# Performance work log

Measured on AMD Instinct MI355X. Metric: run time of the kernel, lower is better.

## Reference

```python
import jax, jax.numpy as jnp
import numpy as np

N_NODES = 100000
N_EDGES = 1600000
IN_DIM, H1, H2, OUT_DIM = 128, 64, 64, 64


def _glorot(key, shape):
    fan_in, fan_out = shape
    lim = np.sqrt(6.0 / (fan_in + fan_out)).astype(np.float32)
    return jax.random.uniform(key, shape, jnp.float32, -lim, lim)


def setup_inputs() -> dict:
    key = jax.random.key(0)
    ks = jax.random.split(key, 8)
    x = jax.random.normal(ks[0], (N_NODES, IN_DIM), jnp.float32)
    edge_index = jax.random.randint(ks[1], (2, N_EDGES), 0, N_NODES, jnp.int64)
    W1 = _glorot(ks[2], (IN_DIM, H1))
    b1 = jnp.zeros((H1,), jnp.float32)
    W2 = _glorot(ks[3], (H1, H2))
    b2 = jnp.zeros((H2,), jnp.float32)
    Wfc = _glorot(ks[4], (H2, OUT_DIM))
    bfc = jnp.zeros((OUT_DIM,), jnp.float32)
    return {"x": x, "W1": W1, "b1": b1, "W2": W2, "b2": b2,
            "Wfc": Wfc, "bfc": bfc, "edge_index": edge_index}


def _gcn_conv(x, src, dst, dinv, W, b, n_nodes):
    # PyG GCNConv: h = D^{-1/2} (A + I) D^{-1/2} (x W) + b
    h = x @ W                                   # [N, out]
    norm = dinv[src] * dinv[dst]                # [E'] edge weights
    msg = norm[:, None] * h[src]                # gather + scale, [E', out]
    agg = jax.ops.segment_sum(msg, dst, num_segments=n_nodes)
    return agg + b


def reference(x, W1, b1, W2, b2, Wfc, bfc, edge_index):
    n = x.shape[0]
    loop = jnp.arange(n, dtype=edge_index.dtype)
    src = jnp.concatenate([edge_index[0], loop])   # self-loops appended
    dst = jnp.concatenate([edge_index[1], loop])
    deg = jnp.zeros((n,), x.dtype).at[dst].add(1.0)  # degree incl. self-loop
    dinv = jax.lax.rsqrt(deg)

    h = jax.nn.relu(_gcn_conv(x, src, dst, dinv, W1, b1, n))
    h = jax.nn.relu(_gcn_conv(h, src, dst, dinv, W2, b2, n))
    embedding = h
    logits = h @ Wfc + bfc
    return embedding, logits
```

## Files before the change

### kernel.cpp

```cpp
#include <hip/hip_runtime.h>
#include <hip/hip_bf16.h>


constexpr int IN_DIM  = 128;
constexpr int HDIM    = 64;
constexpr int NBLK_A  = 256;
constexpr int BSH     = 8;
constexpr int MAXNB   = 512;
constexpr int PADSLK  = 1792;

__device__ __forceinline__ float bf2f(unsigned int u) {
    return __uint_as_float(u << 16);
}
__device__ __forceinline__ unsigned short f2bf_bits(float f) {
    __hip_bfloat16 b = __float2bfloat16(f);
    return *(unsigned short*)&b;
}


__global__ void binA_count(const int* __restrict__ dst, int* __restrict__ histg,
                           int E, int NB, int chunk) {
    __shared__ int h[MAXNB];
    for (int i = threadIdx.x; i < NB; i += 256) h[i] = 0;
    __syncthreads();
    int beg = blockIdx.x * chunk;
    int end = min(E, beg + chunk);
    for (int e = beg + threadIdx.x; e < end; e += 256)
        atomicAdd(&h[dst[e] >> BSH], 1);
    __syncthreads();
    for (int i = threadIdx.x; i < NB; i += 256)
        histg[i * NBLK_A + blockIdx.x] = h[i];
}

__global__ void binA_scanblocks(int* __restrict__ histg, int* __restrict__ btot) {
    __shared__ int sm[NBLK_A];
    int tid = threadIdx.x;
    int v = histg[blockIdx.x * NBLK_A + tid];
    sm[tid] = v;
    __syncthreads();
    for (int off = 1; off < NBLK_A; off <<= 1) {
        int t = (tid >= off) ? sm[tid - off] : 0;
        __syncthreads();
        sm[tid] += t;
        __syncthreads();
    }
    histg[blockIdx.x * NBLK_A + tid] = sm[tid] - v;
    if (tid == NBLK_A - 1) btot[blockIdx.x] = sm[tid];
}

__device__ __forceinline__ void bucket_scan(const int* __restrict__ btot,
                                            int* bb, int NB) {
    int tid = threadIdx.x;
    for (int i = tid; i < MAXNB; i += 256) bb[i] = (i < NB) ? btot[i] : 0;
    __syncthreads();
    for (int off = 1; off < MAXNB; off <<= 1) {
        int i0 = tid, i1 = tid + 256;
        int t0 = (i0 >= off) ? bb[i0 - off] : 0;
        int t1 = (i1 >= off) ? bb[i1 - off] : 0;
        __syncthreads();
        bb[i0] += t0;
        bb[i1] += t1;
        __syncthreads();
    }
}

__global__ void binA_scatter(const int* __restrict__ src, const int* __restrict__ dst,
                             const int* __restrict__ histg, const int* __restrict__ btot,
                             int* __restrict__ staging, int E, int NB, int chunk) {
    __shared__ int bb[MAXNB];
    __shared__ int cur[MAXNB];
    bucket_scan(btot, bb, NB);
    for (int i = threadIdx.x; i < NB; i += 256)
        cur[i] = (bb[i] - btot[i]) + histg[i * NBLK_A + blockIdx.x];
    __syncthreads();
    int beg = blockIdx.x * chunk;
    int end = min(E, beg + chunk);
    for (int e = beg + threadIdx.x; e < end; e += 256) {
        int s = src[e];
        int d = dst[e];
        int pos = atomicAdd(&cur[d >> BSH], 1);
        staging[pos] = (s << BSH) | (d & 255);
    }
}

__global__ void binB_finalize(const int* __restrict__ staging, const int* __restrict__ btot,
                              int2* __restrict__ rows, int* __restrict__ esrc,
                              float* __restrict__ dinv, unsigned int* __restrict__ hp_rowN,
                              int N, int NB) {
    __shared__ int bb[MAXNB];
    __shared__ int cnt[256], sm[256], cur[256];
    int tid = threadIdx.x;
    int b = blockIdx.x;
    bucket_scan(btot, bb, NB);
    int node0 = b << BSH;
    int nloc = min(256, N - node0);
    int eend = bb[b];
    int ebeg = eend - btot[b];
    int ebegP = ebeg + b * PADSLK;
    cnt[tid] = 0;
    __syncthreads();
    for (int e = ebeg + tid; e < eend; e += 256)
        atomicAdd(&cnt[staging[e] & 255], 1);
    __syncthreads();
    int v = cnt[tid];
    int pv = (v + 7) & ~7;
    sm[tid] = pv;
    __syncthreads();
    for (int off = 1; off < 256; off <<= 1) {
        int t = (tid >= off) ? sm[tid - off] : 0;
        __syncthreads();
        sm[tid] += t;
        __syncthreads();
    }
    int excl = sm[tid] - pv;
    cur[tid] = excl;
    __syncthreads();
    if (tid < nloc) {
        rows[node0 + tid] = make_int2(ebegP + excl, ebegP + excl + pv);
        dinv[node0 + tid] = rsqrtf((float)v + 1.0f);
        for (int q = v; q < pv; ++q)
            esrc[ebegP + excl + q] = N;
    }
    if (b == 0 && tid < 32) hp_rowN[tid] = 0u;
    for (int e = ebeg + tid; e < eend; e += 256) {
        int p = staging[e];
        int pos = ebegP + atomicAdd(&cur[p & 255], 1);
        esrc[pos] = p >> BSH;
    }
}


template<int K, bool IBF16, bool SCALE, bool BIAS, bool OBF16>
__device__ __forceinline__ void gemm_body(
        const void* __restrict__ Xv, const float* __restrict__ W,
        const float* __restrict__ bias, const float* __restrict__ dinv,
        void* __restrict__ Yv, int n) {
    constexpr int KC = 32;
    constexpr int XSTR = 132;
    __shared__ float Xt[KC * XSTR];
    __shared__ float Ws[KC * 64];
    const int tid = threadIdx.x;
    const int node0 = blockIdx.x * 128;
    const int r0 = (tid >> 4) * 8;
    const int c0 = (tid & 15) * 4;

    float acc[8][4];
#pragma unroll
    for (int a = 0; a < 8; ++a)
#pragma unroll
        for (int b = 0; b < 4; ++b) acc[a][b] = 0.f;

    for (int kc = 0; kc < K; kc += KC) {
        __syncthreads();
#pragma unroll
        for (int i = 0; i < 4; ++i) {
            int s = tid + i * 256;
            int row = s >> 3;
            int kq = s & 7;
            int grow = node0 + row;
            float4 v = make_float4(0.f, 0.f, 0.f, 0.f);
            if (grow < n) {
                if (IBF16) {
                    uint2 u = *(const uint2*)&((const unsigned short*)Xv)[(size_t)grow * K + kc + kq * 4];
                    v.x = bf2f(u.x & 0xffff); v.y = bf2f(u.x >> 16);
                    v.z = bf2f(u.y & 0xffff); v.w = bf2f(u.y >> 16);
                } else {
                    v = *(const float4*)&((const float*)Xv)[(size_t)grow * K + kc + kq * 4];
                }
            }
            Xt[(kq * 4 + 0) * XSTR + row] = v.x;
            Xt[(kq * 4 + 1) * XSTR + row] = v.y;
            Xt[(kq * 4 + 2) * XSTR + row] = v.z;
            Xt[(kq * 4 + 3) * XSTR + row] = v.w;
        }
#pragma unroll
        for (int i = 0; i < 2; ++i) {
            int s = tid + i * 256;
            *(float4*)&Ws[s * 4] = *(const float4*)&W[(size_t)kc * 64 + s * 4];
        }
        __syncthreads();
#pragma unroll
        for (int kk = 0; kk < KC; kk += 4) {
            float4 xa[4][2];
            float4 wv[4];
#pragma unroll
            for (int i = 0; i < 4; ++i) {
                xa[i][0] = *(const float4*)&Xt[(kk + i) * XSTR + r0];
                xa[i][1] = *(const float4*)&Xt[(kk + i) * XSTR + r0 + 4];
                wv[i]    = *(const float4*)&Ws[(kk + i) * 64 + c0];
            }
#pragma unroll
            for (int i = 0; i < 4; ++i) {
                const float* xp = (const float*)&xa[i][0];
                const float* wp = (const float*)&wv[i];
#pragma unroll
                for (int rr = 0; rr < 8; ++rr)
#pragma unroll
                    for (int cc = 0; cc < 4; ++cc)
                        acc[rr][cc] += xp[rr] * wp[cc];
            }
        }
    }
#pragma unroll
    for (int rr = 0; rr < 8; ++rr) {
        int node = node0 + r0 + rr;
        if (node < n) {
            float d = SCALE ? dinv[node] : 1.0f;
            float t[4];
#pragma unroll
            for (int cc = 0; cc < 4; ++cc) {
                float v = acc[rr][cc];
                if (BIAS) v += bias[c0 + cc];
                t[cc] = v * d;
            }
            if (OBF16) {
                __hip_bfloat16 vb[4];
#pragma unroll
                for (int cc = 0; cc < 4; ++cc) vb[cc] = __float2bfloat16(t[cc]);
                *(uint2*)&((__hip_bfloat16*)Yv)[(size_t)node * 64 + c0] = *(uint2*)vb;
            } else {
                *(float4*)&((float*)Yv)[(size_t)node * 64 + c0] = *(float4*)t;
            }
        }
    }
}

__global__ __launch_bounds__(256, 4) void gemm1_kernel(
        const float* X, const float* W, const float* dinv, void* Y, int n) {
    gemm_body<IN_DIM, false, true, false, true>(X, W, nullptr, dinv, Y, n);
}
__global__ __launch_bounds__(256, 4) void gemm2_kernel(
        const void* X, const float* W, const float* dinv, void* Y, int n) {
    gemm_body<HDIM, true, true, false, true>(X, W, nullptr, dinv, Y, n);
}
__global__ __launch_bounds__(256, 4) void fc_kernel(
        const float* X, const float* W, const float* bias, void* Y, int n) {
    gemm_body<HDIM, false, false, true, false>(X, W, bias, nullptr, Y, n);
}

template<bool OBF16>
__global__ __launch_bounds__(256) void agg_kernel(
        const uint4* __restrict__ hp4, const int* __restrict__ esrc,
        const int2* __restrict__ rows, const float* __restrict__ dinv,
        const float* __restrict__ bias, void* __restrict__ out, int n) {
    const int lane = threadIdx.x & 63;
    const int j = lane & 7;
    const int step = gridDim.x * 32;
    for (int idx = blockIdx.x * 32 + (threadIdx.x >> 6) * 8 + (lane >> 3);
         idx < n; idx += step) {
        const int node = idx;
        const int2 be = rows[node];

        float acc[8];
        {
            uint4 u = hp4[(size_t)node * 8 + j];
            acc[0] = bf2f(u.x & 0xffff); acc[1] = bf2f(u.x >> 16);
            acc[2] = bf2f(u.y & 0xffff); acc[3] = bf2f(u.y >> 16);
            acc[4] = bf2f(u.z & 0xffff); acc[5] = bf2f(u.z >> 16);
            acc[6] = bf2f(u.w & 0xffff); acc[7] = bf2f(u.w >> 16);
        }
        int k = be.x;
        for (; k + 16 <= be.y; k += 16) {
            int s[16];
#pragma unroll
            for (int i = 0; i < 16; ++i)
                s[i] = __builtin_nontemporal_load(&esrc[k + i]);
            uint4 u[16];
#pragma unroll
            for (int i = 0; i < 16; ++i)
                u[i] = hp4[(size_t)s[i] * 8 + j];
#pragma unroll
            for (int i = 0; i < 16; ++i) {
                acc[0] += bf2f(u[i].x & 0xffff); acc[1] += bf2f(u[i].x >> 16);
                acc[2] += bf2f(u[i].y & 0xffff); acc[3] += bf2f(u[i].y >> 16);
                acc[4] += bf2f(u[i].z & 0xffff); acc[5] += bf2f(u[i].z >> 16);
                acc[6] += bf2f(u[i].w & 0xffff); acc[7] += bf2f(u[i].w >> 16);
            }
        }
        if (k < be.y) {
            int s[8];
#pragma unroll
            for (int i = 0; i < 8; ++i)
                s[i] = __builtin_nontemporal_load(&esrc[k + i]);
            uint4 u[8];
#pragma unroll
            for (int i = 0; i < 8; ++i)
                u[i] = hp4[(size_t)s[i] * 8 + j];
#pragma unroll
            for (int i = 0; i < 8; ++i) {
                acc[0] += bf2f(u[i].x & 0xffff); acc[1] += bf2f(u[i].x >> 16);
                acc[2] += bf2f(u[i].y & 0xffff); acc[3] += bf2f(u[i].y >> 16);
                acc[4] += bf2f(u[i].z & 0xffff); acc[5] += bf2f(u[i].z >> 16);
                acc[6] += bf2f(u[i].w & 0xffff); acc[7] += bf2f(u[i].w >> 16);
            }
        }
        const float d = dinv[node];
        float o[8];
#pragma unroll
        for (int t = 0; t < 8; ++t)
            o[t] = fmaxf(fmaf(d, acc[t], bias[8 * j + t]), 0.f);

        if (OBF16) {
            uint4 pk;
            pk.x = (unsigned)f2bf_bits(o[0]) | ((unsigned)f2bf_bits(o[1]) << 16);
            pk.y = (unsigned)f2bf_bits(o[2]) | ((unsigned)f2bf_bits(o[3]) << 16);
            pk.z = (unsigned)f2bf_bits(o[4]) | ((unsigned)f2bf_bits(o[5]) << 16);
            pk.w = (unsigned)f2bf_bits(o[6]) | ((unsigned)f2bf_bits(o[7]) << 16);
            ((uint4*)out)[(size_t)node * 8 + j] = pk;
        } else {
            ((float4*)out)[(size_t)node * 16 + 2 * j]     = make_float4(o[0], o[1], o[2], o[3]);
            ((float4*)out)[(size_t)node * 16 + 2 * j + 1] = make_float4(o[4], o[5], o[6], o[7]);
        }
    }
}

extern "C" void kernel_launch(void* const* d_in, const int* in_sizes, int n_in,
                              void* d_out, int out_size, void* d_ws, size_t ws_size,
                              hipStream_t stream) {
    const float* x   = (const float*)d_in[0];
    const float* W1  = (const float*)d_in[1];
    const float* b1  = (const float*)d_in[2];
    const float* W2  = (const float*)d_in[3];
    const float* b2  = (const float*)d_in[4];
    const float* Wfc = (const float*)d_in[5];
    const float* bfc = (const float*)d_in[6];
    const int*  eidx = (const int*)d_in[7];

    const int N = in_sizes[0] / IN_DIM;
    const int E = in_sizes[7] / 2;
    const int* src = eidx;
    const int* dst = eidx + E;

    const int NB    = (N + 255) >> BSH;
    const int chunk = (E + NBLK_A - 1) / NBLK_A;
    const int EP    = E + NB * PADSLK;

    int* p = (int*)d_ws;
    int2* rows = (int2*)p;           p += (size_t)2 * N + 2;
    float* dinv = (float*)p;         p += (size_t)((N + 3) & ~3);
    int* histg = p;                  p += (size_t)((NB * NBLK_A + 3) & ~3);
    int* btot = p;                   p += 512;
    int* esrc = p;                   p += (size_t)((EP + 3) & ~3);
    unsigned short* hp = (unsigned short*)p;   p += (size_t)(N + 1) * 32;
    unsigned short* h1 = (unsigned short*)p;   p += (size_t)N * 32;
    int* staging = (int*)hp;
    unsigned int* hp_rowN = (unsigned int*)(hp + (size_t)N * 64);

    float* emb    = (float*)d_out;
    float* logits = emb + (size_t)N * HDIM;

    binA_count<<<NBLK_A, 256, 0, stream>>>(dst, histg, E, NB, chunk);
    binA_scanblocks<<<NB, NBLK_A, 0, stream>>>(histg, btot);
    binA_scatter<<<NBLK_A, 256, 0, stream>>>(src, dst, histg, btot, staging, E, NB, chunk);
    binB_finalize<<<NB, 256, 0, stream>>>(staging, btot, rows, esrc, dinv, hp_rowN, N, NB);

    const int gBlocks = (N + 127) / 128;
    const int aBlocks = 2048;

    gemm1_kernel<<<gBlocks, 256, 0, stream>>>(x, W1, dinv, hp, N);
    agg_kernel<true><<<aBlocks, 256, 0, stream>>>(
        (const uint4*)hp, esrc, rows, dinv, b1, h1, N);

    gemm2_kernel<<<gBlocks, 256, 0, stream>>>(h1, W2, dinv, hp, N);
    agg_kernel<false><<<aBlocks, 256, 0, stream>>>(
        (const uint4*)hp, esrc, rows, dinv, b2, emb, N);

    fc_kernel<<<gBlocks, 256, 0, stream>>>(emb, Wfc, bfc, logits, N);
}
```

Measured before the change: 314.8 us.

## Fuse next-layer GEMM and FC into aggregation kernels

The layer-2 GEMM and the final FC layer are folded into the epilogues of the two aggregation kernels. Each 8-lane group writes its aggregated row to shared memory and multiplies it by a weight matrix held in LDS, which removes two kernel launches and the round trips of h1 and the embedding through global memory. A second padded bf16 buffer is added for layer-2 features, and the 16-wide unrolled gather loop is dropped in favour of the 8-wide one. The cost is 16KB+ of shared memory per block, which may reduce occupancy of the memory-bound gather, plus redundant per-node matmul work done on CUDA cores.

```diff
diff --git a/kernel.cpp b/kernel.cpp
--- a/kernel.cpp
+++ b/kernel.cpp
@@ -86,7 +86,7 @@
 __global__ void binB_finalize(const int* __restrict__ staging, const int* __restrict__ btot,
                               int2* __restrict__ rows, int* __restrict__ esrc,
                               float* __restrict__ dinv, unsigned int* __restrict__ hp_rowN,
-                              int N, int NB) {
+                              unsigned int* __restrict__ hp2_rowN, int N, int NB) {
     __shared__ int bb[MAXNB];
     __shared__ int cnt[256], sm[256], cur[256];
     int tid = threadIdx.x;
@@ -121,7 +121,10 @@
         for (int q = v; q < pv; ++q)
             esrc[ebegP + excl + q] = N;
     }
-    if (b == 0 && tid < 32) hp_rowN[tid] = 0u;
+    if (b == 0 && tid < 32) {
+        hp_rowN[tid] = 0u;
+        hp2_rowN[tid] = 0u;
+    }
     for (int e = ebeg + tid; e < eend; e += 256) {
         int p = staging[e];
         int pos = ebegP + atomicAdd(&cur[p & 255], 1);
@@ -130,11 +133,10 @@
 }
 
 
-template<int K, bool IBF16, bool SCALE, bool BIAS, bool OBF16>
-__device__ __forceinline__ void gemm_body(
-        const void* __restrict__ Xv, const float* __restrict__ W,
-        const float* __restrict__ bias, const float* __restrict__ dinv,
-        void* __restrict__ Yv, int n) {
+__global__ __launch_bounds__(256, 4) void gemm1_kernel(
+        const float* __restrict__ X, const float* __restrict__ W,
+        const float* __restrict__ dinv, unsigned short* __restrict__ Y, int n) {
+    constexpr int K = IN_DIM;
     constexpr int KC = 32;
     constexpr int XSTR = 132;
     __shared__ float Xt[KC * XSTR];
@@ -159,15 +161,8 @@
             int kq = s & 7;
             int grow = node0 + row;
             float4 v = make_float4(0.f, 0.f, 0.f, 0.f);
-            if (grow < n) {
-                if (IBF16) {
-                    uint2 u = *(const uint2*)&((const unsigned short*)Xv)[(size_t)grow * K + kc + kq * 4];
-                    v.x = bf2f(u.x & 0xffff); v.y = bf2f(u.x >> 16);
-                    v.z = bf2f(u.y & 0xffff); v.w = bf2f(u.y >> 16);
-                } else {
-                    v = *(const float4*)&((const float*)Xv)[(size_t)grow * K + kc + kq * 4];
-                }
-            }
+            if (grow < n)
+                v = *(const float4*)&X[(size_t)grow * K + kc + kq * 4];
             Xt[(kq * 4 + 0) * XSTR + row] = v.x;
             Xt[(kq * 4 + 1) * XSTR + row] = v.y;
             Xt[(kq * 4 + 2) * XSTR + row] = v.z;
@@ -205,79 +200,56 @@
     for (int rr = 0; rr < 8; ++rr) {
         int node = node0 + r0 + rr;
         if (node < n) {
-            float d = SCALE ? dinv[node] : 1.0f;
-            float t[4];
-#pragma unroll
-            for (int cc = 0; cc < 4; ++cc) {
-                float v = acc[rr][cc];
-                if (BIAS) v += bias[c0 + cc];
-                t[cc] = v * d;
-            }
-            if (OBF16) {
-                __hip_bfloat16 vb[4];
-#pragma unroll
-                for (int cc = 0; cc < 4; ++cc) vb[cc] = __float2bfloat16(t[cc]);
-                *(uint2*)&((__hip_bfloat16*)Yv)[(size_t)node * 64 + c0] = *(uint2*)vb;
-            } else {
-                *(float4*)&((float*)Yv)[(size_t)node * 64 + c0] = *(float4*)t;
-            }
-        }
-    }
-}
-
-__global__ __launch_bounds__(256, 4) void gemm1_kernel(
-        const float* X, const float* W, const float* dinv, void* Y, int n) {
-    gemm_body<IN_DIM, false, true, false, true>(X, W, nullptr, dinv, Y, n);
-}
-__global__ __launch_bounds__(256, 4) void gemm2_kernel(
-        const void* X, const float* W, const float* dinv, void* Y, int n) {
-    gemm_body<HDIM, true, true, false, true>(X, W, nullptr, dinv, Y, n);
-}
-__global__ __launch_bounds__(256, 4) void fc_kernel(
-        const float* X, const float* W, const float* bias, void* Y, int n) {
-    gemm_body<HDIM, false, false, true, false>(X, W, bias, nullptr, Y, n);
-}
-
-template<bool OBF16>
-__global__ __launch_bounds__(256) void agg_kernel(
+            float d = dinv[node];
+            __hip_bfloat16 vb[4];
+#pragma unroll
+            for (int cc = 0; cc < 4; ++cc)
+                vb[cc] = __float2bfloat16(acc[rr][cc] * d);
+            *(uint2*)&Y[(size_t)node * 64 + c0] = *(uint2*)vb;
+        }
+    }
+}
+
+template<int MODE>
+__global__ __launch_bounds__(256) void agg_fused(
         const uint4* __restrict__ hp4, const int* __restrict__ esrc,
         const int2* __restrict__ rows, const float* __restrict__ dinv,
-        const float* __restrict__ bias, void* __restrict__ out, int n) {
+        const float* __restrict__ bias, const float* __restrict__ Wn,
+        const float* __restrict__ bfc, void* __restrict__ out,
+        float* __restrict__ logits, int n) {
+    __shared__ float Ws[64 * 64];
+    __shared__ float rb[4][8][68];
+    for (int i = threadIdx.x; i < 1024; i += 256)
+        ((float4*)Ws)[i] = ((const float4*)Wn)[i];
+    __syncthreads();
+
     const int lane = threadIdx.x & 63;
     const int j = lane & 7;
+    const int g = lane >> 3;
+    const int w = threadIdx.x >> 6;
     const int step = gridDim.x * 32;
-    for (int idx = blockIdx.x * 32 + (threadIdx.x >> 6) * 8 + (lane >> 3);
-         idx < n; idx += step) {
-        const int node = idx;
-        const int2 be = rows[node];
+
+    float bb0[8];
+#pragma unroll
+    for (int t = 0; t < 8; ++t) bb0[t] = bias[8 * j + t];
+    float bo[8];
+    if (MODE == 1) {
+#pragma unroll
+        for (int t = 0; t < 8; ++t) bo[t] = bfc[8 * j + t];
+    }
+
+    for (int idx = blockIdx.x * 32 + w * 8 + g; idx < n; idx += step) {
+        const int2 be = rows[idx];
 
         float acc[8];
         {
-            uint4 u = hp4[(size_t)node * 8 + j];
+            uint4 u = hp4[(size_t)idx * 8 + j];
             acc[0] = bf2f(u.x & 0xffff); acc[1] = bf2f(u.x >> 16);
             acc[2] = bf2f(u.y & 0xffff); acc[3] = bf2f(u.y >> 16);
             acc[4] = bf2f(u.z & 0xffff); acc[5] = bf2f(u.z >> 16);
             acc[6] = bf2f(u.w & 0xffff); acc[7] = bf2f(u.w >> 16);
         }
-        int k = be.x;
-        for (; k + 16 <= be.y; k += 16) {
-            int s[16];
-#pragma unroll
-            for (int i = 0; i < 16; ++i)
-                s[i] = __builtin_nontemporal_load(&esrc[k + i]);
-            uint4 u[16];
-#pragma unroll
-            for (int i = 0; i < 16; ++i)
-                u[i] = hp4[(size_t)s[i] * 8 + j];
-#pragma unroll
-            for (int i = 0; i < 16; ++i) {
-                acc[0] += bf2f(u[i].x & 0xffff); acc[1] += bf2f(u[i].x >> 16);
-                acc[2] += bf2f(u[i].y & 0xffff); acc[3] += bf2f(u[i].y >> 16);
-                acc[4] += bf2f(u[i].z & 0xffff); acc[5] += bf2f(u[i].z >> 16);
-                acc[6] += bf2f(u[i].w & 0xffff); acc[7] += bf2f(u[i].w >> 16);
-            }
-        }
-        if (k < be.y) {
+        for (int k = be.x; k < be.y; k += 8) {
             int s[8];
 #pragma unroll
             for (int i = 0; i < 8; ++i)
@@ -294,22 +266,47 @@
                 acc[6] += bf2f(u[i].w & 0xffff); acc[7] += bf2f(u[i].w >> 16);
             }
         }
-        const float d = dinv[node];
+        const float d = dinv[idx];
         float o[8];
 #pragma unroll
         for (int t = 0; t < 8; ++t)
-            o[t] = fmaxf(fmaf(d, acc[t], bias[8 * j + t]), 0.f);
-
-        if (OBF16) {
+            o[t] = fmaxf(fmaf(d, acc[t], bb0[t]), 0.f);
+
+        *(float4*)&rb[w][g][j * 8]     = make_float4(o[0], o[1], o[2], o[3]);
+        *(float4*)&rb[w][g][j * 8 + 4] = make_float4(o[4], o[5], o[6], o[7]);
+
+        float y[8] = {0.f, 0.f, 0.f, 0.f, 0.f, 0.f, 0.f, 0.f};
+#pragma unroll
+        for (int fw = 0; fw < 8; ++fw) {
+            float4 r0 = *(const float4*)&rb[w][g][fw * 8];
+            float4 r1 = *(const float4*)&rb[w][g][fw * 8 + 4];
+            float rv[8] = {r0.x, r0.y, r0.z, r0.w, r1.x, r1.y, r1.z, r1.w};
+#pragma unroll
+            for (int e = 0; e < 8; ++e) {
+                float val = rv[e];
+                const float4 w0 = *(const float4*)&Ws[(fw * 8 + e) * 64 + j * 8];
+                const float4 w1 = *(const float4*)&Ws[(fw * 8 + e) * 64 + j * 8 + 4];
+                y[0] = fmaf(val, w0.x, y[0]); y[1] = fmaf(val, w0.y, y[1]);
+                y[2] = fmaf(val, w0.z, y[2]); y[3] = fmaf(val, w0.w, y[3]);
+                y[4] = fmaf(val, w1.x, y[4]); y[5] = fmaf(val, w1.y, y[5]);
+                y[6] = fmaf(val, w1.z, y[6]); y[7] = fmaf(val, w1.w, y[7]);
+            }
+        }
+
+        if (MODE == 0) {
             uint4 pk;
-            pk.x = (unsigned)f2bf_bits(o[0]) | ((unsigned)f2bf_bits(o[1]) << 16);
-            pk.y = (unsigned)f2bf_bits(o[2]) | ((unsigned)f2bf_bits(o[3]) << 16);
-            pk.z = (unsigned)f2bf_bits(o[4]) | ((unsigned)f2bf_bits(o[5]) << 16);
-            pk.w = (unsigned)f2bf_bits(o[6]) | ((unsigned)f2bf_bits(o[7]) << 16);
-            ((uint4*)out)[(size_t)node * 8 + j] = pk;
+            pk.x = (unsigned)f2bf_bits(y[0] * d) | ((unsigned)f2bf_bits(y[1] * d) << 16);
+            pk.y = (unsigned)f2bf_bits(y[2] * d) | ((unsigned)f2bf_bits(y[3] * d) << 16);
+            pk.z = (unsigned)f2bf_bits(y[4] * d) | ((unsigned)f2bf_bits(y[5] * d) << 16);
+            pk.w = (unsigned)f2bf_bits(y[6] * d) | ((unsigned)f2bf_bits(y[7] * d) << 16);
+            ((uint4*)out)[(size_t)idx * 8 + j] = pk;
         } else {
-            ((float4*)out)[(size_t)node * 16 + 2 * j]     = make_float4(o[0], o[1], o[2], o[3]);
-            ((float4*)out)[(size_t)node * 16 + 2 * j + 1] = make_float4(o[4], o[5], o[6], o[7]);
+            ((float4*)out)[(size_t)idx * 16 + 2 * j]     = make_float4(o[0], o[1], o[2], o[3]);
+            ((float4*)out)[(size_t)idx * 16 + 2 * j + 1] = make_float4(o[4], o[5], o[6], o[7]);
+            float4 l0 = make_float4(y[0] + bo[0], y[1] + bo[1], y[2] + bo[2], y[3] + bo[3]);
+            float4 l1 = make_float4(y[4] + bo[4], y[5] + bo[5], y[6] + bo[6], y[7] + bo[7]);
+            *(float4*)&logits[(size_t)idx * 64 + 8 * j]     = l0;
+            *(float4*)&logits[(size_t)idx * 64 + 8 * j + 4] = l1;
         }
     }
 }
@@ -341,10 +338,11 @@
     int* histg = p;                  p += (size_t)((NB * NBLK_A + 3) & ~3);
     int* btot = p;                   p += 512;
     int* esrc = p;                   p += (size_t)((EP + 3) & ~3);
-    unsigned short* hp = (unsigned short*)p;   p += (size_t)(N + 1) * 32;
-    unsigned short* h1 = (unsigned short*)p;   p += (size_t)N * 32;
+    unsigned short* hp  = (unsigned short*)p;  p += (size_t)(N + 1) * 32;
+    unsigned short* hp2 = (unsigned short*)p;  p += (size_t)(N + 1) * 32;
     int* staging = (int*)hp;
-    unsigned int* hp_rowN = (unsigned int*)(hp + (size_t)N * 64);
+    unsigned int* hp_rowN  = (unsigned int*)(hp  + (size_t)N * 64);
+    unsigned int* hp2_rowN = (unsigned int*)(hp2 + (size_t)N * 64);
 
     float* emb    = (float*)d_out;
     float* logits = emb + (size_t)N * HDIM;
@@ -352,18 +350,17 @@
     binA_count<<<NBLK_A, 256, 0, stream>>>(dst, histg, E, NB, chunk);
     binA_scanblocks<<<NB, NBLK_A, 0, stream>>>(histg, btot);
     binA_scatter<<<NBLK_A, 256, 0, stream>>>(src, dst, histg, btot, staging, E, NB, chunk);
-    binB_finalize<<<NB, 256, 0, stream>>>(staging, btot, rows, esrc, dinv, hp_rowN, N, NB);
+    binB_finalize<<<NB, 256, 0, stream>>>(staging, btot, rows, esrc, dinv,
+                                          hp_rowN, hp2_rowN, N, NB);
 
     const int gBlocks = (N + 127) / 128;
     const int aBlocks = 2048;
 
     gemm1_kernel<<<gBlocks, 256, 0, stream>>>(x, W1, dinv, hp, N);
-    agg_kernel<true><<<aBlocks, 256, 0, stream>>>(
-        (const uint4*)hp, esrc, rows, dinv, b1, h1, N);
-
-    gemm2_kernel<<<gBlocks, 256, 0, stream>>>(h1, W2, dinv, hp, N);
-    agg_kernel<false><<<aBlocks, 256, 0, stream>>>(
-        (const uint4*)hp, esrc, rows, dinv, b2, emb, N);
-
-    fc_kernel<<<gBlocks, 256, 0, stream>>>(emb, Wfc, bfc, logits, N);
-}
+
+    agg_fused<0><<<aBlocks, 256, 0, stream>>>(
+        (const uint4*)hp, esrc, rows, dinv, b1, W2, nullptr, hp2, nullptr, N);
+
+    agg_fused<1><<<aBlocks, 256, 0, stream>>>(
+        (const uint4*)hp2, esrc, rows, dinv, b2, Wfc, bfc, emb, logits, N);
+}
```

Result: slower. 405.2 us (+28.7%).

## Replace two-level bucketed CSR build with atomic histogram and fused scatter

Applied to the files above, without the earlier changes.

Replaces the four-kernel bucket-sort CSR construction with a global degree histogram built by atomics, a wave-level scan that hands out row slots through an atomic counter, and an edge scatter using per-node atomic cursors. The scatter is folded into the first GEMM launch as extra blocks, so edge placement can overlap with the dense transform. Rows are no longer in node order and edges within a row land in nondeterministic order, which can hurt gather locality in aggregation and makes summation order vary between runs. Global atomics on 1.6M edges replace the shared-memory atomics used before.

```diff
diff --git a/kernel.cpp b/kernel.cpp
--- a/kernel.cpp
+++ b/kernel.cpp
@@ -4,10 +4,7 @@
 
 constexpr int IN_DIM  = 128;
 constexpr int HDIM    = 64;
-constexpr int NBLK_A  = 256;
-constexpr int BSH     = 8;
-constexpr int MAXNB   = 512;
-constexpr int PADSLK  = 1792;
+constexpr int SB      = 256;
 
 __device__ __forceinline__ float bf2f(unsigned int u) {
     return __uint_as_float(u << 16);
@@ -18,114 +15,44 @@
 }
 
 
-__global__ void binA_count(const int* __restrict__ dst, int* __restrict__ histg,
-                           int E, int NB, int chunk) {
-    __shared__ int h[MAXNB];
-    for (int i = threadIdx.x; i < NB; i += 256) h[i] = 0;
-    __syncthreads();
-    int beg = blockIdx.x * chunk;
-    int end = min(E, beg + chunk);
-    for (int e = beg + threadIdx.x; e < end; e += 256)
-        atomicAdd(&h[dst[e] >> BSH], 1);
-    __syncthreads();
-    for (int i = threadIdx.x; i < NB; i += 256)
-        histg[i * NBLK_A + blockIdx.x] = h[i];
-}
-
-__global__ void binA_scanblocks(int* __restrict__ histg, int* __restrict__ btot) {
-    __shared__ int sm[NBLK_A];
-    int tid = threadIdx.x;
-    int v = histg[blockIdx.x * NBLK_A + tid];
-    sm[tid] = v;
-    __syncthreads();
-    for (int off = 1; off < NBLK_A; off <<= 1) {
-        int t = (tid >= off) ? sm[tid - off] : 0;
-        __syncthreads();
-        sm[tid] += t;
-        __syncthreads();
-    }
-    histg[blockIdx.x * NBLK_A + tid] = sm[tid] - v;
-    if (tid == NBLK_A - 1) btot[blockIdx.x] = sm[tid];
-}
-
-__device__ __forceinline__ void bucket_scan(const int* __restrict__ btot,
-                                            int* bb, int NB) {
-    int tid = threadIdx.x;
-    for (int i = tid; i < MAXNB; i += 256) bb[i] = (i < NB) ? btot[i] : 0;
-    __syncthreads();
-    for (int off = 1; off < MAXNB; off <<= 1) {
-        int i0 = tid, i1 = tid + 256;
-        int t0 = (i0 >= off) ? bb[i0 - off] : 0;
-        int t1 = (i1 >= off) ? bb[i1 - off] : 0;
-        __syncthreads();
-        bb[i0] += t0;
-        bb[i1] += t1;
-        __syncthreads();
-    }
-}
-
-__global__ void binA_scatter(const int* __restrict__ src, const int* __restrict__ dst,
-                             const int* __restrict__ histg, const int* __restrict__ btot,
-                             int* __restrict__ staging, int E, int NB, int chunk) {
-    __shared__ int bb[MAXNB];
-    __shared__ int cur[MAXNB];
-    bucket_scan(btot, bb, NB);
-    for (int i = threadIdx.x; i < NB; i += 256)
-        cur[i] = (bb[i] - btot[i]) + histg[i * NBLK_A + blockIdx.x];
-    __syncthreads();
-    int beg = blockIdx.x * chunk;
-    int end = min(E, beg + chunk);
-    for (int e = beg + threadIdx.x; e < end; e += 256) {
-        int s = src[e];
-        int d = dst[e];
-        int pos = atomicAdd(&cur[d >> BSH], 1);
-        staging[pos] = (s << BSH) | (d & 255);
-    }
-}
-
-__global__ void binB_finalize(const int* __restrict__ staging, const int* __restrict__ btot,
-                              int2* __restrict__ rows, int* __restrict__ esrc,
-                              float* __restrict__ dinv, unsigned int* __restrict__ hp_rowN,
-                              int N, int NB) {
-    __shared__ int bb[MAXNB];
-    __shared__ int cnt[256], sm[256], cur[256];
-    int tid = threadIdx.x;
-    int b = blockIdx.x;
-    bucket_scan(btot, bb, NB);
-    int node0 = b << BSH;
-    int nloc = min(256, N - node0);
-    int eend = bb[b];
-    int ebeg = eend - btot[b];
-    int ebegP = ebeg + b * PADSLK;
-    cnt[tid] = 0;
-    __syncthreads();
-    for (int e = ebeg + tid; e < eend; e += 256)
-        atomicAdd(&cnt[staging[e] & 255], 1);
-    __syncthreads();
-    int v = cnt[tid];
-    int pv = (v + 7) & ~7;
-    sm[tid] = pv;
-    __syncthreads();
-    for (int off = 1; off < 256; off <<= 1) {
-        int t = (tid >= off) ? sm[tid - off] : 0;
-        __syncthreads();
-        sm[tid] += t;
-        __syncthreads();
-    }
-    int excl = sm[tid] - pv;
-    cur[tid] = excl;
-    __syncthreads();
-    if (tid < nloc) {
-        rows[node0 + tid] = make_int2(ebegP + excl, ebegP + excl + pv);
-        dinv[node0 + tid] = rsqrtf((float)v + 1.0f);
-        for (int q = v; q < pv; ++q)
-            esrc[ebegP + excl + q] = N;
-    }
-    if (b == 0 && tid < 32) hp_rowN[tid] = 0u;
-    for (int e = ebeg + tid; e < eend; e += 256) {
-        int p = staging[e];
-        int pos = ebegP + atomicAdd(&cur[p & 255], 1);
-        esrc[pos] = p >> BSH;
+__global__ void zero_kernel(int* __restrict__ deg, int* __restrict__ total,
+                            unsigned int* __restrict__ hp_rowN, int N) {
+    int i = blockIdx.x * 256 + threadIdx.x;
+    int step = gridDim.x * 256;
+    for (; i < N; i += step) deg[i] = 0;
+    if (blockIdx.x == 0 && threadIdx.x == 0) *total = 0;
+    if (blockIdx.x == 1 && threadIdx.x < 32) hp_rowN[threadIdx.x] = 0u;
+}
+
+__global__ void hist_kernel(const int* __restrict__ dst, int* __restrict__ deg, int E) {
+    int i = blockIdx.x * 256 + threadIdx.x;
+    int step = gridDim.x * 256;
+    for (; i < E; i += step) atomicAdd(&deg[dst[i]], 1);
+}
+
+__global__ void alloc_kernel(const int* __restrict__ deg, int* __restrict__ total,
+                             int2* __restrict__ rows, int* __restrict__ cur,
+                             float* __restrict__ dinv, int* __restrict__ esrc, int N) {
+    int idx = blockIdx.x * 256 + threadIdx.x;
+    int lane = threadIdx.x & 63;
+    int dg = (idx < N) ? deg[idx] : 0;
+    int pv = (dg + 7) & ~7;
+    int incl = pv;
+#pragma unroll
+    for (int off = 1; off < 64; off <<= 1) {
+        int t = __shfl_up(incl, off, 64);
+        if (lane >= off) incl += t;
+    }
+    int wtot = __shfl(incl, 63, 64);
+    int base = 0;
+    if (lane == 63) base = atomicAdd(total, wtot);
+    base = __shfl(base, 63, 64);
+    int start = base + incl - pv;
+    if (idx < N) {
+        rows[idx] = make_int2(start, start + pv);
+        cur[idx] = start;
+        dinv[idx] = rsqrtf((float)dg + 1.0f);
+        for (int q = dg; q < pv; ++q) esrc[start + q] = N;
     }
 }
 
@@ -134,13 +61,13 @@
 __device__ __forceinline__ void gemm_body(
         const void* __restrict__ Xv, const float* __restrict__ W,
         const float* __restrict__ bias, const float* __restrict__ dinv,
-        void* __restrict__ Yv, int n) {
+        void* __restrict__ Yv, int n, int bid) {
     constexpr int KC = 32;
     constexpr int XSTR = 132;
     __shared__ float Xt[KC * XSTR];
     __shared__ float Ws[KC * 64];
     const int tid = threadIdx.x;
-    const int node0 = blockIdx.x * 128;
+    const int node0 = bid * 128;
     const int r0 = (tid >> 4) * 8;
     const int c0 = (tid & 15) * 4;
 
@@ -225,18 +152,33 @@
     }
 }
 
-__global__ __launch_bounds__(256, 4) void gemm1_kernel(
-        const float* X, const float* W, const float* dinv, void* Y, int n) {
-    gemm_body<IN_DIM, false, true, false, true>(X, W, nullptr, dinv, Y, n);
-}
+__global__ __launch_bounds__(256, 4) void gemm1_scatter_kernel(
+        const float* __restrict__ X, const float* __restrict__ W,
+        const float* __restrict__ dinv, unsigned short* __restrict__ Y,
+        const int* __restrict__ src, const int* __restrict__ dst,
+        int* __restrict__ cur, int* __restrict__ esrc, int gB, int E, int n) {
+    if ((int)blockIdx.x >= gB) {
+        int i = ((int)blockIdx.x - gB) * 256 + threadIdx.x;
+        int step = SB * 256;
+        for (; i < E; i += step) {
+            int d = dst[i];
+            int p = atomicAdd(&cur[d], 1);
+            esrc[p] = src[i];
+        }
+        return;
+    }
+    gemm_body<IN_DIM, false, true, false, true>(X, W, nullptr, dinv, Y, n, blockIdx.x);
+}
+
 __global__ __launch_bounds__(256, 4) void gemm2_kernel(
         const void* X, const float* W, const float* dinv, void* Y, int n) {
-    gemm_body<HDIM, true, true, false, true>(X, W, nullptr, dinv, Y, n);
+    gemm_body<HDIM, true, true, false, true>(X, W, nullptr, dinv, Y, n, blockIdx.x);
 }
 __global__ __launch_bounds__(256, 4) void fc_kernel(
         const float* X, const float* W, const float* bias, void* Y, int n) {
-    gemm_body<HDIM, false, false, true, false>(X, W, bias, nullptr, Y, n);
-}
+    gemm_body<HDIM, false, false, true, false>(X, W, bias, nullptr, Y, n, blockIdx.x);
+}
+
 
 template<bool OBF16>
 __global__ __launch_bounds__(256) void agg_kernel(
@@ -331,39 +273,38 @@
     const int* src = eidx;
     const int* dst = eidx + E;
 
-    const int NB    = (N + 255) >> BSH;
-    const int chunk = (E + NBLK_A - 1) / NBLK_A;
-    const int EP    = E + NB * PADSLK;
+    const int EP = E + 7 * ((N + 7) & ~7) + 16;
 
     int* p = (int*)d_ws;
     int2* rows = (int2*)p;           p += (size_t)2 * N + 2;
     float* dinv = (float*)p;         p += (size_t)((N + 3) & ~3);
-    int* histg = p;                  p += (size_t)((NB * NBLK_A + 3) & ~3);
-    int* btot = p;                   p += 512;
+    int* deg = p;                    p += (size_t)((N + 3) & ~3);
+    int* cur = p;                    p += (size_t)((N + 3) & ~3);
+    int* total = p;                  p += 4;
     int* esrc = p;                   p += (size_t)((EP + 3) & ~3);
     unsigned short* hp = (unsigned short*)p;   p += (size_t)(N + 1) * 32;
     unsigned short* h1 = (unsigned short*)p;   p += (size_t)N * 32;
-    int* staging = (int*)hp;
     unsigned int* hp_rowN = (unsigned int*)(hp + (size_t)N * 64);
 
     float* emb    = (float*)d_out;
     float* logits = emb + (size_t)N * HDIM;
 
-    binA_count<<<NBLK_A, 256, 0, stream>>>(dst, histg, E, NB, chunk);
-    binA_scanblocks<<<NB, NBLK_A, 0, stream>>>(histg, btot);
-    binA_scatter<<<NBLK_A, 256, 0, stream>>>(src, dst, histg, btot, staging, E, NB, chunk);
-    binB_finalize<<<NB, 256, 0, stream>>>(staging, btot, rows, esrc, dinv, hp_rowN, N, NB);
-
-    const int gBlocks = (N + 127) / 128;
+    const int gB = (N + 127) / 128;
     const int aBlocks = 2048;
 
-    gemm1_kernel<<<gBlocks, 256, 0, stream>>>(x, W1, dinv, hp, N);
+    zero_kernel<<<256, 256, 0, stream>>>(deg, total, hp_rowN, N);
+    hist_kernel<<<512, 256, 0, stream>>>(dst, deg, E);
+    alloc_kernel<<<(N + 255) / 256, 256, 0, stream>>>(deg, total, rows, cur, dinv, esrc, N);
+
+    gemm1_scatter_kernel<<<gB + SB, 256, 0, stream>>>(
+        x, W1, dinv, hp, src, dst, cur, esrc, gB, E, N);
+
     agg_kernel<true><<<aBlocks, 256, 0, stream>>>(
         (const uint4*)hp, esrc, rows, dinv, b1, h1, N);
 
-    gemm2_kernel<<<gBlocks, 256, 0, stream>>>(h1, W2, dinv, hp, N);
+    gemm2_kernel<<<gB, 256, 0, stream>>>(h1, W2, dinv, hp, N);
     agg_kernel<false><<<aBlocks, 256, 0, stream>>>(
         (const uint4*)hp, esrc, rows, dinv, b2, emb, N);
 
-    fc_kernel<<<gBlocks, 256, 0, stream>>>(emb, Wfc, bfc, logits, N);
-}
+    fc_kernel<<<gB, 256, 0, stream>>>(emb, Wfc, bfc, logits, N);
+}
```

New measurement: 413.1 us. +31.2%, slower.

## Co-schedule first GEMM with edge binning kernels and move dinv scaling into finalize

Applied to the files above, without the earlier changes.

Splits the first-layer GEMM into two halves and runs each half inside the same launch as the histogram-count and scatter binning blocks, so the dense compute overlaps the edge sort. The separate block-scan kernel is dropped. Bucket totals are now accumulated with global atomics, and each scatter block sums the previous blocks' histograms serially to find its offsets. Because dinv is not known during GEMM1, the dinv row scaling moves into binB_finalize as an extra bf16 read-modify-write pass over hp. Staging gets its own buffer and a memset is added. The costs are a second rounding of hp and the serial prefix loop in the scatter blocks.

```diff
diff --git a/kernel.cpp b/kernel.cpp
--- a/kernel.cpp
+++ b/kernel.cpp
@@ -7,6 +7,7 @@
 constexpr int NBLK_A  = 256;
 constexpr int BSH     = 8;
 constexpr int MAXNB   = 512;
+constexpr int HISTW   = 512;
 constexpr int PADSLK  = 1792;
 
 __device__ __forceinline__ float bf2f(unsigned int u) {
@@ -15,37 +16,6 @@
 __device__ __forceinline__ unsigned short f2bf_bits(float f) {
     __hip_bfloat16 b = __float2bfloat16(f);
     return *(unsigned short*)&b;
-}
-
-
-__global__ void binA_count(const int* __restrict__ dst, int* __restrict__ histg,
-                           int E, int NB, int chunk) {
-    __shared__ int h[MAXNB];
-    for (int i = threadIdx.x; i < NB; i += 256) h[i] = 0;
-    __syncthreads();
-    int beg = blockIdx.x * chunk;
-    int end = min(E, beg + chunk);
-    for (int e = beg + threadIdx.x; e < end; e += 256)
-        atomicAdd(&h[dst[e] >> BSH], 1);
-    __syncthreads();
-    for (int i = threadIdx.x; i < NB; i += 256)
-        histg[i * NBLK_A + blockIdx.x] = h[i];
-}
-
-__global__ void binA_scanblocks(int* __restrict__ histg, int* __restrict__ btot) {
-    __shared__ int sm[NBLK_A];
-    int tid = threadIdx.x;
-    int v = histg[blockIdx.x * NBLK_A + tid];
-    sm[tid] = v;
-    __syncthreads();
-    for (int off = 1; off < NBLK_A; off <<= 1) {
-        int t = (tid >= off) ? sm[tid - off] : 0;
-        __syncthreads();
-        sm[tid] += t;
-        __syncthreads();
-    }
-    histg[blockIdx.x * NBLK_A + tid] = sm[tid] - v;
-    if (tid == NBLK_A - 1) btot[blockIdx.x] = sm[tid];
 }
 
 __device__ __forceinline__ void bucket_scan(const int* __restrict__ btot,
@@ -64,83 +34,18 @@
     }
 }
 
-__global__ void binA_scatter(const int* __restrict__ src, const int* __restrict__ dst,
-                             const int* __restrict__ histg, const int* __restrict__ btot,
-                             int* __restrict__ staging, int E, int NB, int chunk) {
-    __shared__ int bb[MAXNB];
-    __shared__ int cur[MAXNB];
-    bucket_scan(btot, bb, NB);
-    for (int i = threadIdx.x; i < NB; i += 256)
-        cur[i] = (bb[i] - btot[i]) + histg[i * NBLK_A + blockIdx.x];
-    __syncthreads();
-    int beg = blockIdx.x * chunk;
-    int end = min(E, beg + chunk);
-    for (int e = beg + threadIdx.x; e < end; e += 256) {
-        int s = src[e];
-        int d = dst[e];
-        int pos = atomicAdd(&cur[d >> BSH], 1);
-        staging[pos] = (s << BSH) | (d & 255);
-    }
-}
-
-__global__ void binB_finalize(const int* __restrict__ staging, const int* __restrict__ btot,
-                              int2* __restrict__ rows, int* __restrict__ esrc,
-                              float* __restrict__ dinv, unsigned int* __restrict__ hp_rowN,
-                              int N, int NB) {
-    __shared__ int bb[MAXNB];
-    __shared__ int cnt[256], sm[256], cur[256];
-    int tid = threadIdx.x;
-    int b = blockIdx.x;
-    bucket_scan(btot, bb, NB);
-    int node0 = b << BSH;
-    int nloc = min(256, N - node0);
-    int eend = bb[b];
-    int ebeg = eend - btot[b];
-    int ebegP = ebeg + b * PADSLK;
-    cnt[tid] = 0;
-    __syncthreads();
-    for (int e = ebeg + tid; e < eend; e += 256)
-        atomicAdd(&cnt[staging[e] & 255], 1);
-    __syncthreads();
-    int v = cnt[tid];
-    int pv = (v + 7) & ~7;
-    sm[tid] = pv;
-    __syncthreads();
-    for (int off = 1; off < 256; off <<= 1) {
-        int t = (tid >= off) ? sm[tid - off] : 0;
-        __syncthreads();
-        sm[tid] += t;
-        __syncthreads();
-    }
-    int excl = sm[tid] - pv;
-    cur[tid] = excl;
-    __syncthreads();
-    if (tid < nloc) {
-        rows[node0 + tid] = make_int2(ebegP + excl, ebegP + excl + pv);
-        dinv[node0 + tid] = rsqrtf((float)v + 1.0f);
-        for (int q = v; q < pv; ++q)
-            esrc[ebegP + excl + q] = N;
-    }
-    if (b == 0 && tid < 32) hp_rowN[tid] = 0u;
-    for (int e = ebeg + tid; e < eend; e += 256) {
-        int p = staging[e];
-        int pos = ebegP + atomicAdd(&cur[p & 255], 1);
-        esrc[pos] = p >> BSH;
-    }
-}
-
 
 template<int K, bool IBF16, bool SCALE, bool BIAS, bool OBF16>
 __device__ __forceinline__ void gemm_body(
         const void* __restrict__ Xv, const float* __restrict__ W,
         const float* __restrict__ bias, const float* __restrict__ dinv,
-        void* __restrict__ Yv, int n) {
+        void* __restrict__ Yv, int n, int bid) {
     constexpr int KC = 32;
     constexpr int XSTR = 132;
     __shared__ float Xt[KC * XSTR];
     __shared__ float Ws[KC * 64];
     const int tid = threadIdx.x;
-    const int node0 = blockIdx.x * 128;
+    const int node0 = bid * 128;
     const int r0 = (tid >> 4) * 8;
     const int c0 = (tid & 15) * 4;
 
@@ -225,18 +130,137 @@
     }
 }
 
-__global__ __launch_bounds__(256, 4) void gemm1_kernel(
-        const float* X, const float* W, const float* dinv, void* Y, int n) {
-    gemm_body<IN_DIM, false, true, false, true>(X, W, nullptr, dinv, Y, n);
-}
+__global__ __launch_bounds__(256, 4) void gemm1_count_kernel(
+        const float* __restrict__ X, const float* __restrict__ W,
+        unsigned short* __restrict__ Y,
+        const int* __restrict__ dst, int* __restrict__ histg, int* __restrict__ btot,
+        int gB2, int E, int NB, int chunk, int n) {
+    if ((int)blockIdx.x >= gB2) {
+        int cbid = (int)blockIdx.x - gB2;
+        __shared__ int h[HISTW];
+        for (int i = threadIdx.x; i < HISTW; i += 256) h[i] = 0;
+        __syncthreads();
+        int beg = cbid * chunk;
+        int end = min(E, beg + chunk);
+        for (int e = beg + threadIdx.x; e < end; e += 256)
+            atomicAdd(&h[dst[e] >> BSH], 1);
+        __syncthreads();
+        for (int i = threadIdx.x; i < HISTW; i += 256) {
+            int v = h[i];
+            histg[cbid * HISTW + i] = v;
+            if (v) atomicAdd(&btot[i], v);
+        }
+        return;
+    }
+    gemm_body<IN_DIM, false, false, false, true>(X, W, nullptr, nullptr, Y, n, blockIdx.x);
+}
+
+__global__ __launch_bounds__(256, 4) void gemm1_scatter_kernel(
+        const float* __restrict__ X, const float* __restrict__ W,
+        unsigned short* __restrict__ Y,
+        const int* __restrict__ src, const int* __restrict__ dst,
+        const int* __restrict__ histg, const int* __restrict__ btot,
+        int* __restrict__ staging, int gB1b, int gB2, int E, int NB, int chunk, int n) {
+    if ((int)blockIdx.x >= gB1b) {
+        int B = (int)blockIdx.x - gB1b;
+        __shared__ int bb[MAXNB];
+        __shared__ int cur[MAXNB];
+        bucket_scan(btot, bb, NB);
+        for (int t = threadIdx.x; t < HISTW; t += 256) {
+            int s = bb[t] - btot[t];
+            for (int r = 0; r < B; ++r) s += histg[r * HISTW + t];
+            cur[t] = s;
+        }
+        __syncthreads();
+        int beg = B * chunk;
+        int end = min(E, beg + chunk);
+        for (int e = beg + threadIdx.x; e < end; e += 256) {
+            int s = src[e];
+            int d = dst[e];
+            int pos = atomicAdd(&cur[d >> BSH], 1);
+            staging[pos] = (s << BSH) | (d & 255);
+        }
+        return;
+    }
+    gemm_body<IN_DIM, false, false, false, true>(X, W, nullptr, nullptr, Y, n,
+                                                 gB2 + (int)blockIdx.x);
+}
+
+__global__ void binB_finalize(const int* __restrict__ staging, const int* __restrict__ btot,
+                              int2* __restrict__ rows, int* __restrict__ esrc,
+                              float* __restrict__ dinv, uint4* __restrict__ hp4,
+                              int N, int NB) {
+    __shared__ int bb[MAXNB];
+    __shared__ int cnt[256], sm[256], cur[256];
+    __shared__ float dls[256];
+    int tid = threadIdx.x;
+    int b = blockIdx.x;
+    bucket_scan(btot, bb, NB);
+    int node0 = b << BSH;
+    int nloc = min(256, N - node0);
+    int eend = bb[b];
+    int ebeg = eend - btot[b];
+    int ebegP = ebeg + b * PADSLK;
+    cnt[tid] = 0;
+    dls[tid] = 1.0f;
+    __syncthreads();
+    for (int e = ebeg + tid; e < eend; e += 256)
+        atomicAdd(&cnt[staging[e] & 255], 1);
+    __syncthreads();
+    int v = cnt[tid];
+    int pv = (v + 7) & ~7;
+    sm[tid] = pv;
+    __syncthreads();
+    for (int off = 1; off < 256; off <<= 1) {
+        int t = (tid >= off) ? sm[tid - off] : 0;
+        __syncthreads();
+        sm[tid] += t;
+        __syncthreads();
+    }
+    int excl = sm[tid] - pv;
+    cur[tid] = excl;
+    __syncthreads();
+    if (tid < nloc) {
+        float d = rsqrtf((float)v + 1.0f);
+        rows[node0 + tid] = make_int2(ebegP + excl, ebegP + excl + pv);
+        dinv[node0 + tid] = d;
+        dls[tid] = d;
+        for (int q = v; q < pv; ++q)
+            esrc[ebegP + excl + q] = N;
+    }
+    if (b == 0 && tid < 8) hp4[(size_t)N * 8 + tid] = make_uint4(0, 0, 0, 0);
+    for (int e = ebeg + tid; e < eend; e += 256) {
+        int p = staging[e];
+        int pos = ebegP + atomicAdd(&cur[p & 255], 1);
+        esrc[pos] = p >> BSH;
+    }
+    __syncthreads();
+    int m = nloc * 8;
+    uint4* hpq = hp4 + (size_t)node0 * 8;
+    for (int q = tid; q < m; q += 256) {
+        float dd = dls[q >> 3];
+        uint4 u = hpq[q];
+        unsigned int r[4];
+        const unsigned int* up = &u.x;
+#pragma unroll
+        for (int c = 0; c < 4; ++c) {
+            float lo = bf2f(up[c] & 0xffff) * dd;
+            float hi = bf2f(up[c] >> 16) * dd;
+            r[c] = (unsigned)f2bf_bits(lo) | ((unsigned)f2bf_bits(hi) << 16);
+        }
+        hpq[q] = make_uint4(r[0], r[1], r[2], r[3]);
+    }
+}
+
 __global__ __launch_bounds__(256, 4) void gemm2_kernel(
         const void* X, const float* W, const float* dinv, void* Y, int n) {
-    gemm_body<HDIM, true, true, false, true>(X, W, nullptr, dinv, Y, n);
+    gemm_body<HDIM, true, true, false, true>(X, W, nullptr, dinv, Y, n, blockIdx.x);
 }
 __global__ __launch_bounds__(256, 4) void fc_kernel(
         const float* X, const float* W, const float* bias, void* Y, int n) {
-    gemm_body<HDIM, false, false, true, false>(X, W, bias, nullptr, Y, n);
-}
+    gemm_body<HDIM, false, false, true, false>(X, W, bias, nullptr, Y, n, blockIdx.x);
+}
+
 
 template<bool OBF16>
 __global__ __launch_bounds__(256) void agg_kernel(
@@ -338,32 +362,38 @@
     int* p = (int*)d_ws;
     int2* rows = (int2*)p;           p += (size_t)2 * N + 2;
     float* dinv = (float*)p;         p += (size_t)((N + 3) & ~3);
-    int* histg = p;                  p += (size_t)((NB * NBLK_A + 3) & ~3);
+    int* histg = p;                  p += (size_t)NBLK_A * HISTW;
     int* btot = p;                   p += 512;
+    int* staging = p;                p += (size_t)((E + 3) & ~3);
     int* esrc = p;                   p += (size_t)((EP + 3) & ~3);
     unsigned short* hp = (unsigned short*)p;   p += (size_t)(N + 1) * 32;
     unsigned short* h1 = (unsigned short*)p;   p += (size_t)N * 32;
-    int* staging = (int*)hp;
-    unsigned int* hp_rowN = (unsigned int*)(hp + (size_t)N * 64);
 
     float* emb    = (float*)d_out;
     float* logits = emb + (size_t)N * HDIM;
 
-    binA_count<<<NBLK_A, 256, 0, stream>>>(dst, histg, E, NB, chunk);
-    binA_scanblocks<<<NB, NBLK_A, 0, stream>>>(histg, btot);
-    binA_scatter<<<NBLK_A, 256, 0, stream>>>(src, dst, histg, btot, staging, E, NB, chunk);
-    binB_finalize<<<NB, 256, 0, stream>>>(staging, btot, rows, esrc, dinv, hp_rowN, N, NB);
-
-    const int gBlocks = (N + 127) / 128;
+    const int gB  = (N + 127) / 128;
+    const int gB2 = (gB + 1) / 2;
+    const int gB1b = gB - gB2;
     const int aBlocks = 2048;
 
-    gemm1_kernel<<<gBlocks, 256, 0, stream>>>(x, W1, dinv, hp, N);
+    hipMemsetAsync(btot, 0, 512 * sizeof(int), stream);
+
+    gemm1_count_kernel<<<gB2 + NBLK_A, 256, 0, stream>>>(
+        x, W1, hp, dst, histg, btot, gB2, E, NB, chunk, N);
+
+    gemm1_scatter_kernel<<<gB1b + NBLK_A, 256, 0, stream>>>(
+        x, W1, hp, src, dst, histg, btot, staging, gB1b, gB2, E, NB, chunk, N);
+
+    binB_finalize<<<NB, 256, 0, stream>>>(staging, btot, rows, esrc, dinv,
+                                          (uint4*)hp, N, NB);
+
     agg_kernel<true><<<aBlocks, 256, 0, stream>>>(
         (const uint4*)hp, esrc, rows, dinv, b1, h1, N);
 
-    gemm2_kernel<<<gBlocks, 256, 0, stream>>>(h1, W2, dinv, hp, N);
+    gemm2_kernel<<<gB, 256, 0, stream>>>(h1, W2, dinv, hp, N);
     agg_kernel<false><<<aBlocks, 256, 0, stream>>>(
         (const uint4*)hp, esrc, rows, dinv, b2, emb, N);
 
-    fc_kernel<<<gBlocks, 256, 0, stream>>>(emb, Wfc, bfc, logits, N);
-}
+    fc_kernel<<<gB, 256, 0, stream>>>(emb, Wfc, bfc, logits, N);
+}
```

Result: slower. 350.1 us (+11.2%).
